# Performance work log

Hardware: AMD Instinct MI355X
Metric: run time of the kernel (lower is better)

The kernel has to match this reference:

```python
import jax, jax.numpy as jnp
import numpy as np

B, S, D, R = 8, 2048, 2048, 256


def soft_threshold24(w):
    """2:4 soft-threshold: in each contiguous group of 4 along the last dim,
    keep the top-2 |w| and shrink them by the 3rd-largest |w| (soft threshold),
    zeroing the bottom two. Mirrors soft_threshold24_triton."""
    rows, K = w.shape
    g = w.reshape(rows, K // 4, 4)
    a = jnp.abs(g)
    t = jnp.sort(a, axis=-1)[..., 1:2]  # 2nd smallest == 3rd largest per group
    sp = jnp.sign(g) * jnp.maximum(a - t, 0.0)
    return sp.reshape(rows, K)


def fp16_mm(a, b):
    """fake_fp8_mm: cast operands to fp16, matmul with fp32 accumulation/output."""
    return jnp.matmul(a.astype(jnp.float16), b.astype(jnp.float16),
                      preferred_element_type=jnp.float32)


def sparse_linear(x, w, b, scale):
    """SparseOverlayFunction.forward: 2:4-sparsified, scaled weight + fp16 GEMM."""
    x2 = x.reshape(-1, x.shape[-1])                # [N, K]
    ws = soft_threshold24(w) * scale               # [K, M], 2:4 sparse * learnable scale
    out = fp16_mm(x2, ws)                          # [N, M] fp32
    out = out.reshape(x.shape[:-1] + (w.shape[-1],))
    return out + b


def setup_inputs():
    key = jax.random.key(0)
    ks = jax.random.split(key, 4)
    x = jax.random.normal(ks[0], (B, S, D), jnp.float32)
    weight_in = jax.random.normal(ks[1], (D, R), jnp.float32) * 0.02
    weight_out = jax.random.normal(ks[2], (R, D), jnp.float32) * 0.02
    bias_in = jnp.zeros((R,), jnp.float32)
    bias_out = jax.random.normal(ks[3], (D,), jnp.float32) * 0.01
    sparse_scale_in = jnp.ones((1,), jnp.float32)
    sparse_scale_out = jnp.ones((1,), jnp.float32)
    return {"x": x, "weight_in": weight_in, "weight_out": weight_out,
            "bias_in": bias_in, "bias_out": bias_out,
            "sparse_scale_in": sparse_scale_in, "sparse_scale_out": sparse_scale_out}


def reference(x, weight_in, weight_out, bias_in, bias_out, sparse_scale_in, sparse_scale_out):
    h = sparse_linear(x, weight_in, bias_in, sparse_scale_in)    # [B,S,R]
    y = sparse_linear(h, weight_out, bias_out, sparse_scale_out)  # [B,S,D]
    return y
```

## Files before the change

### kernel.cpp

```cpp
#include <hip/hip_runtime.h>
#include <stdint.h>
#include <stddef.h>

typedef _Float16 f16;
typedef __attribute__((ext_vector_type(8))) _Float16 f16x8;
typedef __attribute__((ext_vector_type(4))) float f32x4;

#define GPTR(p) ((const __attribute__((address_space(1))) void*)(p))
#define LPTR(p) ((__attribute__((address_space(3))) void*)(p))

__device__ __forceinline__ void async16(const void* g, void* l) {
    __builtin_amdgcn_global_load_lds(GPTR(g), LPTR(l), 16, 0, 0);
}

#define VMCNT(N) asm volatile("s_waitcnt vmcnt(" #N ")" ::: "memory")
#define SBAR()   do { __builtin_amdgcn_sched_barrier(0); \
                      __builtin_amdgcn_s_barrier();      \
                      __builtin_amdgcn_sched_barrier(0); } while (0)

__global__ __launch_bounds__(256) void sparsify_t_tiled(
        const float* __restrict__ W, const float* __restrict__ scale,
        f16* __restrict__ Wt, int K, int M) {
    __shared__ f16 T[64][80];
    const int r0 = blockIdx.y << 6, m0 = blockIdx.x << 6;
    const float s = scale[0];
    const int t = threadIdx.x;
    const int rr = t >> 2, mb = (t & 3) << 4;
    const float* src = W + (size_t)(r0 + rr) * M + m0 + mb;
    #pragma unroll
    for (int j = 0; j < 4; j++) {
        float4 v = *(const float4*)(src + j * 4);
        float a0 = fabsf(v.x), a1 = fabsf(v.y), a2 = fabsf(v.z), a3 = fabsf(v.w);
        float lo1 = fminf(a0, a1), hi1 = fmaxf(a0, a1);
        float lo2 = fminf(a2, a3), hi2 = fmaxf(a2, a3);
        float th = fminf(fmaxf(lo1, lo2), fminf(hi1, hi2));
        int m = mb + j * 4;
        T[m + 0][rr] = (f16)(copysignf(fmaxf(a0 - th, 0.f), v.x) * s);
        T[m + 1][rr] = (f16)(copysignf(fmaxf(a1 - th, 0.f), v.y) * s);
        T[m + 2][rr] = (f16)(copysignf(fmaxf(a2 - th, 0.f), v.z) * s);
        T[m + 3][rr] = (f16)(copysignf(fmaxf(a3 - th, 0.f), v.w) * s);
    }
    __syncthreads();
    const int mm = t >> 2, rb = (t & 3) << 4;
    f16* dst = Wt + (size_t)(m0 + mm) * K + r0 + rb;
    *(f16x8*)dst       = *(const f16x8*)&T[mm][rb];
    *(f16x8*)(dst + 8) = *(const f16x8*)&T[mm][rb + 8];
}

__global__ __launch_bounds__(512, 2) void gemm1_kernel(
        const float* __restrict__ A, const f16* __restrict__ Bt,
        const float* __restrict__ bias, f16* __restrict__ H) {
    constexpr int K = 2048, RN = 256, BK = 32, NT = K / BK;
    __shared__ float4 Asf[2][64 * 8];
    __shared__ f16x8  Bs[2][256 * 4];

    const int tid  = threadIdx.x;
    const int lane = tid & 63;
    const int wv   = tid >> 6;
    const int wm   = wv & 1, wn = wv >> 1;
    const int lr   = lane & 15, q = lane >> 4;
    const int row0 = blockIdx.x << 6;

    f32x4 acc[2][4] = {};

    const int La = wv * 64 + lane;
    const int ra = La >> 3, ca = (La & 7) ^ (ra & 7);
    const float* aSrc = A + (size_t)(row0 + ra) * K + ca * 4;
    const int Lb0 = (wv * 2 + 0) * 64 + lane;
    const int Lb1 = (wv * 2 + 1) * 64 + lane;
    const int rb0 = Lb0 >> 2, cb0 = (Lb0 & 3) ^ (rb0 & 3);
    const int rb1 = Lb1 >> 2, cb1 = (Lb1 & 3) ^ (rb1 & 3);
    const f16* bSrc0 = Bt + (size_t)rb0 * K + cb0 * 8;
    const f16* bSrc1 = Bt + (size_t)rb1 * K + cb1 * 8;

    auto stage = [&](int k0, int b) {
        async16(aSrc + k0,  (char*)(&Asf[b][0]) + wv * 1024);
        async16(bSrc0 + k0, (char*)(&Bs[b][0]) + (wv * 2 + 0) * 1024);
        async16(bSrc1 + k0, (char*)(&Bs[b][0]) + (wv * 2 + 1) * 1024);
    };

    auto compute = [&](int b) {
        f16x8 af[2], bf[4];
        #pragma unroll
        for (int m = 0; m < 2; m++) {
            int r = wm * 32 + m * 16 + lr;
            float4 v0 = Asf[b][r * 8 + ((2 * q)     ^ (r & 7))];
            float4 v1 = Asf[b][r * 8 + ((2 * q + 1) ^ (r & 7))];
            f16x8 h;
            h[0] = (f16)v0.x; h[1] = (f16)v0.y; h[2] = (f16)v0.z; h[3] = (f16)v0.w;
            h[4] = (f16)v1.x; h[5] = (f16)v1.y; h[6] = (f16)v1.z; h[7] = (f16)v1.w;
            af[m] = h;
        }
        #pragma unroll
        for (int n = 0; n < 4; n++) {
            int r = wn * 64 + n * 16 + lr;
            bf[n] = Bs[b][r * 4 + (q ^ (r & 3))];
        }
        #pragma unroll
        for (int m = 0; m < 2; m++)
            #pragma unroll
            for (int n = 0; n < 4; n++)
                acc[m][n] = __builtin_amdgcn_mfma_f32_16x16x32_f16(
                    af[m], bf[n], acc[m][n], 0, 0, 0);
    };

    stage(0, 0);
    #pragma unroll 2
    for (int t = 0; t < NT - 1; ++t) {
        stage((t + 1) * BK, (t + 1) & 1);
        VMCNT(3);
        SBAR();
        compute(t & 1);
        SBAR();
    }
    VMCNT(0);
    SBAR();
    compute((NT - 1) & 1);

    #pragma unroll
    for (int m = 0; m < 2; m++) {
        int gr0 = row0 + wm * 32 + m * 16 + q * 4;
        #pragma unroll
        for (int n = 0; n < 4; n++) {
            int gc = wn * 64 + n * 16 + lr;
            float bv = bias[gc];
            #pragma unroll
            for (int r = 0; r < 4; r++)
                H[(size_t)(gr0 + r) * RN + gc] = (f16)(acc[m][n][r] + bv);
        }
    }
}

__global__ __launch_bounds__(512, 2) void gemm2_kernel(
        const f16* __restrict__ Hs, const f16* __restrict__ Bt,
        const float* __restrict__ bias, float* __restrict__ Y) {
    constexpr int K = 256, N = 2048, BK = 32, NT = K / BK;
    __shared__ f16x8 As[2][128 * 4];
    __shared__ f16x8 Bs[2][256 * 4];

    const int tid  = threadIdx.x;
    const int lane = tid & 63;
    const int wv   = tid >> 6;
    const int wm   = wv & 1, wn = wv >> 1;
    const int lr   = lane & 15, q = lane >> 4;
    const int row0 = blockIdx.y << 7;
    const int col0 = blockIdx.x << 8;

    f32x4 acc[4][4] = {};

    const int La = wv * 64 + lane;
    const int ra = La >> 2, ca = (La & 3) ^ (ra & 3);
    const f16* aSrc = Hs + (size_t)(row0 + ra) * K + ca * 8;
    const int Lb0 = (wv * 2 + 0) * 64 + lane;
    const int Lb1 = (wv * 2 + 1) * 64 + lane;
    const int rb0 = Lb0 >> 2, cb0 = (Lb0 & 3) ^ (rb0 & 3);
    const int rb1 = Lb1 >> 2, cb1 = (Lb1 & 3) ^ (rb1 & 3);
    const f16* bSrc0 = Bt + (size_t)(col0 + rb0) * K + cb0 * 8;
    const f16* bSrc1 = Bt + (size_t)(col0 + rb1) * K + cb1 * 8;

    auto stage = [&](int k0, int b) {
        async16(aSrc + k0,  (char*)(&As[b][0]) + wv * 1024);
        async16(bSrc0 + k0, (char*)(&Bs[b][0]) + (wv * 2 + 0) * 1024);
        async16(bSrc1 + k0, (char*)(&Bs[b][0]) + (wv * 2 + 1) * 1024);
    };

    auto compute = [&](int b) {
        f16x8 af[4], bf[4];
        #pragma unroll
        for (int m = 0; m < 4; m++) {
            int r = wm * 64 + m * 16 + lr;
            af[m] = As[b][r * 4 + (q ^ (r & 3))];
        }
        #pragma unroll
        for (int n = 0; n < 4; n++) {
            int r = wn * 64 + n * 16 + lr;
            bf[n] = Bs[b][r * 4 + (q ^ (r & 3))];
        }
        #pragma unroll
        for (int m = 0; m < 4; m++)
            #pragma unroll
            for (int n = 0; n < 4; n++)
                acc[m][n] = __builtin_amdgcn_mfma_f32_16x16x32_f16(
                    af[m], bf[n], acc[m][n], 0, 0, 0);
    };

    stage(0, 0);
    for (int t = 0; t < NT - 1; ++t) {
        stage((t + 1) * BK, (t + 1) & 1);
        VMCNT(3);
        SBAR();
        compute(t & 1);
        SBAR();
    }
    VMCNT(0);
    SBAR();
    compute((NT - 1) & 1);

    #pragma unroll
    for (int m = 0; m < 4; m++) {
        int gr0 = row0 + wm * 64 + m * 16 + q * 4;
        #pragma unroll
        for (int n = 0; n < 4; n++) {
            int gc = col0 + wn * 64 + n * 16 + lr;
            float bv = bias[gc];
            #pragma unroll
            for (int r = 0; r < 4; r++)
                Y[(size_t)(gr0 + r) * N + gc] = acc[m][n][r] + bv;
        }
    }
}

extern "C" void kernel_launch(void* const* d_in, const int* in_sizes, int n_in,
                              void* d_out, int out_size, void* d_ws, size_t ws_size,
                              hipStream_t stream) {
    const float* x  = (const float*)d_in[0];
    const float* w1 = (const float*)d_in[1];
    const float* w2 = (const float*)d_in[2];
    const float* b1 = (const float*)d_in[3];
    const float* b2 = (const float*)d_in[4];
    const float* s1 = (const float*)d_in[5];
    const float* s2 = (const float*)d_in[6];
    float* y = (float*)d_out;

    constexpr int NROWS = 8 * 2048;
    constexpr int D = 2048, R = 256;

    char* ws = (char*)d_ws;
    f16* W1t = (f16*)ws;
    f16* W2t = (f16*)(ws + (size_t)R * D * 2);
    f16* H   = (f16*)(ws + (size_t)R * D * 4);

    hipLaunchKernelGGL(sparsify_t_tiled, dim3(R / 64, D / 64), dim3(256),
                       0, stream, w1, s1, W1t, D, R);
    hipLaunchKernelGGL(sparsify_t_tiled, dim3(D / 64, R / 64), dim3(256),
                       0, stream, w2, s2, W2t, R, D);

    hipLaunchKernelGGL(gemm1_kernel, dim3(NROWS / 64), dim3(512),
                       0, stream, x, W1t, b1, H);

    hipLaunchKernelGGL(gemm2_kernel, dim3(D / 256, NROWS / 128), dim3(512),
                       0, stream, H, W2t, b2, y);
}
```

Measured before the change: 298.6 us.

## Use padded K-blocked layouts for weights and H, triple-buffer gemm1

After: 325.3 us. 1.09x slower.

```diff
diff --git a/kernel.cpp b/kernel.cpp
--- a/kernel.cpp
+++ b/kernel.cpp
@@ -18,9 +18,9 @@
                       __builtin_amdgcn_s_barrier();      \
                       __builtin_amdgcn_sched_barrier(0); } while (0)
 
-__global__ __launch_bounds__(256) void sparsify_t_tiled(
+__global__ __launch_bounds__(256) void sparsify_t_pad(
         const float* __restrict__ W, const float* __restrict__ scale,
-        f16* __restrict__ Wt, int K, int M) {
+        f16* __restrict__ Wp, int K, int M) {
     __shared__ f16 T[64][80];
     const int r0 = blockIdx.y << 6, m0 = blockIdx.x << 6;
     const float s = scale[0];
@@ -42,17 +42,20 @@
     }
     __syncthreads();
     const int mm = t >> 2, rb = (t & 3) << 4;
-    f16* dst = Wt + (size_t)(m0 + mm) * K + r0 + rb;
+    const int k  = r0 + rb;
+    f16* dst = Wp + ((size_t)(k >> 5) * M + (m0 + mm)) * 40 + (k & 31);
     *(f16x8*)dst       = *(const f16x8*)&T[mm][rb];
     *(f16x8*)(dst + 8) = *(const f16x8*)&T[mm][rb + 8];
 }
 
 __global__ __launch_bounds__(512, 2) void gemm1_kernel(
-        const float* __restrict__ A, const f16* __restrict__ Bt,
-        const float* __restrict__ bias, f16* __restrict__ H) {
-    constexpr int K = 2048, RN = 256, BK = 32, NT = K / BK;
-    __shared__ float4 Asf[2][64 * 8];
-    __shared__ f16x8  Bs[2][256 * 4];
+        const float* __restrict__ A, const f16* __restrict__ B1p,
+        const float* __restrict__ bias, f16* __restrict__ Hp) {
+    constexpr int K = 2048, BK = 32, NT = K / BK;
+    constexpr int NROWS = 16384;
+    constexpr int ABYTES = 64 * 144;
+    constexpr int STAGE  = ABYTES + 256 * 80;
+    __shared__ char lds[3][STAGE];
 
     const int tid  = threadIdx.x;
     const int lane = tid & 63;
@@ -63,29 +66,40 @@
 
     f32x4 acc[2][4] = {};
 
-    const int La = wv * 64 + lane;
-    const int ra = La >> 3, ca = (La & 7) ^ (ra & 7);
-    const float* aSrc = A + (size_t)(row0 + ra) * K + ca * 4;
-    const int Lb0 = (wv * 2 + 0) * 64 + lane;
-    const int Lb1 = (wv * 2 + 1) * 64 + lane;
-    const int rb0 = Lb0 >> 2, cb0 = (Lb0 & 3) ^ (rb0 & 3);
-    const int rb1 = Lb1 >> 2, cb1 = (Lb1 & 3) ^ (rb1 & 3);
-    const f16* bSrc0 = Bt + (size_t)rb0 * K + cb0 * 8;
-    const f16* bSrc1 = Bt + (size_t)rb1 * K + cb1 * 8;
-
-    auto stage = [&](int k0, int b) {
-        async16(aSrc + k0,  (char*)(&Asf[b][0]) + wv * 1024);
-        async16(bSrc0 + k0, (char*)(&Bs[b][0]) + (wv * 2 + 0) * 1024);
-        async16(bSrc1 + k0, (char*)(&Bs[b][0]) + (wv * 2 + 1) * 1024);
-    };
-
-    auto compute = [&](int b) {
+    const char* sp[4];
+    size_t step[4];
+    int dg[4];
+    #pragma unroll
+    for (int j = 0; j < 4; j++) {
+        int g = (wv < 5) ? (wv * 4 + j) : (20 + (wv - 5) * 3 + (j < 2 ? j : 2));
+        dg[j] = g * 1024;
+        if (g < 9) {
+            int o = g * 1024 + (lane << 4);
+            int r = o / 144;
+            int w = o - r * 144;
+            if (w >= 128) w = 0;
+            sp[j] = (const char*)(A + (size_t)(row0 + r) * K) + w;
+            step[j] = BK * 4;
+        } else {
+            sp[j] = (const char*)B1p + (size_t)(g - 9) * 1024 + (lane << 4);
+            step[j] = 256 * 80;
+        }
+    }
+
+    auto stage = [&](char* buf) {
+        #pragma unroll
+        for (int j = 0; j < 4; j++) { async16(sp[j], buf + dg[j]); sp[j] += step[j]; }
+    };
+
+    auto compute = [&](const char* buf) {
+        const char* Ab = buf;
+        const char* Bb = buf + ABYTES;
         f16x8 af[2], bf[4];
         #pragma unroll
         for (int m = 0; m < 2; m++) {
             int r = wm * 32 + m * 16 + lr;
-            float4 v0 = Asf[b][r * 8 + ((2 * q)     ^ (r & 7))];
-            float4 v1 = Asf[b][r * 8 + ((2 * q + 1) ^ (r & 7))];
+            const float4* va = (const float4*)(Ab + r * 144 + q * 32);
+            float4 v0 = va[0], v1 = va[1];
             f16x8 h;
             h[0] = (f16)v0.x; h[1] = (f16)v0.y; h[2] = (f16)v0.z; h[3] = (f16)v0.w;
             h[4] = (f16)v1.x; h[5] = (f16)v1.y; h[6] = (f16)v1.z; h[7] = (f16)v1.w;
@@ -94,7 +108,7 @@
         #pragma unroll
         for (int n = 0; n < 4; n++) {
             int r = wn * 64 + n * 16 + lr;
-            bf[n] = Bs[b][r * 4 + (q ^ (r & 3))];
+            bf[n] = *(const f16x8*)(Bb + r * 80 + q * 16);
         }
         #pragma unroll
         for (int m = 0; m < 2; m++)
@@ -104,18 +118,21 @@
                     af[m], bf[n], acc[m][n], 0, 0, 0);
     };
 
-    stage(0, 0);
-    #pragma unroll 2
-    for (int t = 0; t < NT - 1; ++t) {
-        stage((t + 1) * BK, (t + 1) & 1);
-        VMCNT(3);
-        SBAR();
-        compute(t & 1);
-        SBAR();
-    }
-    VMCNT(0);
-    SBAR();
-    compute((NT - 1) & 1);
+    char* p0 = lds[0];
+    char* p1 = lds[1];
+    char* p2 = lds[2];
+    stage(p0);
+    stage(p1);
+    for (int t = 0; t < NT - 2; ++t) {
+        stage(p2);
+        VMCNT(8);
+        SBAR();
+        compute(p0);
+        SBAR();
+        char* tmp = p0; p0 = p1; p1 = p2; p2 = tmp;
+    }
+    VMCNT(4); SBAR(); compute(p0);
+    VMCNT(0); SBAR(); compute(p1);
 
     #pragma unroll
     for (int m = 0; m < 2; m++) {
@@ -124,19 +141,21 @@
         for (int n = 0; n < 4; n++) {
             int gc = wn * 64 + n * 16 + lr;
             float bv = bias[gc];
+            f16* hbase = Hp + (size_t)(gc >> 5) * NROWS * 40 + (gc & 31);
             #pragma unroll
             for (int r = 0; r < 4; r++)
-                H[(size_t)(gr0 + r) * RN + gc] = (f16)(acc[m][n][r] + bv);
+                hbase[(size_t)(gr0 + r) * 40] = (f16)(acc[m][n][r] + bv);
         }
     }
 }
 
 __global__ __launch_bounds__(512, 2) void gemm2_kernel(
-        const f16* __restrict__ Hs, const f16* __restrict__ Bt,
+        const f16* __restrict__ Hp, const f16* __restrict__ B2p,
         const float* __restrict__ bias, float* __restrict__ Y) {
-    constexpr int K = 256, N = 2048, BK = 32, NT = K / BK;
-    __shared__ f16x8 As[2][128 * 4];
-    __shared__ f16x8 Bs[2][256 * 4];
+    constexpr int NROWS = 16384, N = 2048, NT = 8;
+    constexpr int ABYTES = 128 * 80;
+    constexpr int STAGE  = ABYTES + 256 * 80;
+    __shared__ char lds[2][STAGE];
 
     const int tid  = threadIdx.x;
     const int lane = tid & 63;
@@ -148,33 +167,41 @@
 
     f32x4 acc[4][4] = {};
 
-    const int La = wv * 64 + lane;
-    const int ra = La >> 2, ca = (La & 3) ^ (ra & 3);
-    const f16* aSrc = Hs + (size_t)(row0 + ra) * K + ca * 8;
-    const int Lb0 = (wv * 2 + 0) * 64 + lane;
-    const int Lb1 = (wv * 2 + 1) * 64 + lane;
-    const int rb0 = Lb0 >> 2, cb0 = (Lb0 & 3) ^ (rb0 & 3);
-    const int rb1 = Lb1 >> 2, cb1 = (Lb1 & 3) ^ (rb1 & 3);
-    const f16* bSrc0 = Bt + (size_t)(col0 + rb0) * K + cb0 * 8;
-    const f16* bSrc1 = Bt + (size_t)(col0 + rb1) * K + cb1 * 8;
-
-    auto stage = [&](int k0, int b) {
-        async16(aSrc + k0,  (char*)(&As[b][0]) + wv * 1024);
-        async16(bSrc0 + k0, (char*)(&Bs[b][0]) + (wv * 2 + 0) * 1024);
-        async16(bSrc1 + k0, (char*)(&Bs[b][0]) + (wv * 2 + 1) * 1024);
-    };
-
-    auto compute = [&](int b) {
+    const char* sp[4];
+    size_t step[4];
+    int dg[4];
+    #pragma unroll
+    for (int j = 0; j < 4; j++) {
+        int g = (wv < 6) ? (wv * 4 + j) : (24 + (wv - 6) * 3 + (j < 2 ? j : 2));
+        dg[j] = g * 1024;
+        if (g < 10) {
+            sp[j] = (const char*)Hp + (size_t)row0 * 80 + g * 1024 + (lane << 4);
+            step[j] = (size_t)NROWS * 80;
+        } else {
+            sp[j] = (const char*)B2p + (size_t)col0 * 80 + (size_t)(g - 10) * 1024
+                    + (lane << 4);
+            step[j] = (size_t)2048 * 80;
+        }
+    }
+
+    auto stage = [&](char* buf) {
+        #pragma unroll
+        for (int j = 0; j < 4; j++) { async16(sp[j], buf + dg[j]); sp[j] += step[j]; }
+    };
+
+    auto compute = [&](const char* buf) {
+        const char* Ab = buf;
+        const char* Bb = buf + ABYTES;
         f16x8 af[4], bf[4];
         #pragma unroll
         for (int m = 0; m < 4; m++) {
             int r = wm * 64 + m * 16 + lr;
-            af[m] = As[b][r * 4 + (q ^ (r & 3))];
+            af[m] = *(const f16x8*)(Ab + r * 80 + q * 16);
         }
         #pragma unroll
         for (int n = 0; n < 4; n++) {
             int r = wn * 64 + n * 16 + lr;
-            bf[n] = Bs[b][r * 4 + (q ^ (r & 3))];
+            bf[n] = *(const f16x8*)(Bb + r * 80 + q * 16);
         }
         #pragma unroll
         for (int m = 0; m < 4; m++)
@@ -184,17 +211,18 @@
                     af[m], bf[n], acc[m][n], 0, 0, 0);
     };
 
-    stage(0, 0);
+    char* p0 = lds[0];
+    char* p1 = lds[1];
+    stage(p0);
     for (int t = 0; t < NT - 1; ++t) {
-        stage((t + 1) * BK, (t + 1) & 1);
-        VMCNT(3);
-        SBAR();
-        compute(t & 1);
-        SBAR();
-    }
-    VMCNT(0);
-    SBAR();
-    compute((NT - 1) & 1);
+        stage(p1);
+        VMCNT(4);
+        SBAR();
+        compute(p0);
+        SBAR();
+        char* tmp = p0; p0 = p1; p1 = tmp;
+    }
+    VMCNT(0); SBAR(); compute(p0);
 
     #pragma unroll
     for (int m = 0; m < 4; m++) {
@@ -226,18 +254,18 @@
     constexpr int D = 2048, R = 256;
 
     char* ws = (char*)d_ws;
-    f16* W1t = (f16*)ws;
-    f16* W2t = (f16*)(ws + (size_t)R * D * 2);
-    f16* H   = (f16*)(ws + (size_t)R * D * 4);
-
-    hipLaunchKernelGGL(sparsify_t_tiled, dim3(R / 64, D / 64), dim3(256),
-                       0, stream, w1, s1, W1t, D, R);
-    hipLaunchKernelGGL(sparsify_t_tiled, dim3(D / 64, R / 64), dim3(256),
-                       0, stream, w2, s2, W2t, R, D);
+    f16* W1p = (f16*)ws;
+    f16* W2p = (f16*)(ws + (2u << 20));
+    f16* Hp  = (f16*)(ws + (4u << 20));
+
+    hipLaunchKernelGGL(sparsify_t_pad, dim3(R / 64, D / 64), dim3(256),
+                       0, stream, w1, s1, W1p, D, R);
+    hipLaunchKernelGGL(sparsify_t_pad, dim3(D / 64, R / 64), dim3(256),
+                       0, stream, w2, s2, W2p, R, D);
 
     hipLaunchKernelGGL(gemm1_kernel, dim3(NROWS / 64), dim3(512),
-                       0, stream, x, W1t, b1, H);
+                       0, stream, x, W1p, b1, Hp);
 
     hipLaunchKernelGGL(gemm2_kernel, dim3(D / 256, NROWS / 128), dim3(512),
-                       0, stream, H, W2t, b2, y);
-}
+                       0, stream, Hp, W2p, b2, y);
+}
```
